# Kernel tuning notes

Hardware: AMD Instinct MI355X
Metric: run time of the kernel (lower is better)

The kernel has to match this reference:

```python
import jax, jax.numpy as jnp
import numpy as np
from jax import lax

B, R, C, K = 4, 512, 80, 100          # images, rois/img, fg classes, post_nms_top_k
NMS_TH, SCORE_TH = 0.3, 0.1
MEAN = jnp.zeros(4, jnp.float32)       # delta_mean
STD = jnp.ones(4, jnp.float32)         # delta_std
NEG = jnp.float32(-1e9)
DWH_CLIP = jnp.float32(4.135166556742356)  # log(1000/16), standard bbox_xform clip


def setup_inputs() -> dict:
    key = jax.random.key(0)
    k1, k2, k3, k4 = jax.random.split(key, 4)
    x1y1 = jax.random.uniform(k1, (B, R, 2), minval=0.0, maxval=800.0)
    wh = jax.random.uniform(k2, (B, R, 2), minval=16.0, maxval=220.0)
    batch_rois = jnp.concatenate([x1y1, jnp.minimum(x1y1 + wh, 1023.0)], axis=-1)
    bbox_score = jax.random.uniform(k3, (B * R, C + 1, 1, 1), dtype=jnp.float32)
    bbox_deltas = jax.random.normal(k4, (B * R, (C + 1) * 4, 1, 1), dtype=jnp.float32) * 0.2
    im_hw = jnp.full((B, 1, 1, 2), 1024, dtype=jnp.int32)
    return {"batch_rois": batch_rois, "bbox_score": bbox_score,
            "bbox_deltas": bbox_deltas, "im_hw": im_hw}


def _pairwise_iou(b):
    # b: [R, 4] (x1,y1,x2,y2) -> [R, R]
    area = (b[:, 2] - b[:, 0]) * (b[:, 3] - b[:, 1])
    lt = jnp.maximum(b[:, None, :2], b[None, :, :2])
    rb = jnp.minimum(b[:, None, 2:], b[None, :, 2:])
    wh = jnp.maximum(rb - lt, 0.0)
    inter = wh[..., 0] * wh[..., 1]
    return inter / (area[:, None] + area[None, :] - inter + 1e-9)


def _nms_one_class(boxes, scores):
    # boxes: [R,4], scores: [R] -> keep mask + score-sorted boxes/scores
    order = jnp.argsort(-scores)
    b = boxes[order]
    s = scores[order]
    iou = _pairwise_iou(b)  # [R, R]

    def body(sup, i):
        keep_i = jnp.logical_and(jnp.logical_not(sup[i]), s[i] > SCORE_TH)
        new = jnp.where(keep_i, jnp.logical_or(sup, iou[i] > NMS_TH), sup)
        new = new.at[i].set(sup[i])  # never self-suppress
        return new, keep_i

    _, keep = lax.scan(body, jnp.zeros(b.shape[0], bool), jnp.arange(b.shape[0]))
    return keep, b, s


def _decode(rois, deltas, hw):
    # rois: [R,4], deltas: [R,C,4], hw: [2] (h, w) -> decoded boxes [R,C,4]
    d = deltas * STD + MEAN
    w = rois[:, 2] - rois[:, 0]
    h = rois[:, 3] - rois[:, 1]
    cx = rois[:, 0] + 0.5 * w
    cy = rois[:, 1] + 0.5 * h
    dx, dy = d[..., 0], d[..., 1]
    dw = jnp.minimum(d[..., 2], DWH_CLIP)
    dh = jnp.minimum(d[..., 3], DWH_CLIP)
    pcx = dx * w[:, None] + cx[:, None]
    pcy = dy * h[:, None] + cy[:, None]
    pw = w[:, None] * jnp.exp(dw)
    ph = h[:, None] * jnp.exp(dh)
    x1 = jnp.clip(pcx - 0.5 * pw, 0.0, hw[1] - 1.0)
    y1 = jnp.clip(pcy - 0.5 * ph, 0.0, hw[0] - 1.0)
    x2 = jnp.clip(pcx + 0.5 * pw, 0.0, hw[1] - 1.0)
    y2 = jnp.clip(pcy + 0.5 * ph, 0.0, hw[0] - 1.0)
    return jnp.stack([x1, y1, x2, y2], axis=-1)


def reference(batch_rois, bbox_score, bbox_deltas, im_hw):
    scores = bbox_score.reshape(B, R, C + 1)[..., 1:]               # [B,R,C] (skip bg)
    deltas = bbox_deltas.reshape(B, R, C + 1, 4)[:, :, 1:, :]       # [B,R,C,4]
    hw = im_hw.reshape(B, 2).astype(jnp.float32)

    def per_image(rois, sc, dl, hw_i):
        boxes = _decode(rois, dl, hw_i)                              # [R,C,4]
        keep, bs, ss = jax.vmap(_nms_one_class)(
            jnp.swapaxes(boxes, 0, 1), sc.T)                         # [C,R]...
        cls = jnp.broadcast_to(jnp.arange(C, dtype=jnp.float32)[:, None], (C, R))
        flat_s = jnp.where(keep, ss, NEG).reshape(-1)                # [C*R]
        top_s, idx = lax.top_k(flat_s, K)
        tb = bs.reshape(-1, 4)[idx]
        tc = cls.reshape(-1)[idx]
        valid = top_s > NEG * 0.5
        row = jnp.concatenate([tb, top_s[:, None], tc[:, None]], axis=-1)  # [K,6]
        pad = jnp.concatenate([jnp.zeros((K, 5), jnp.float32),
                               -jnp.ones((K, 1), jnp.float32)], axis=-1)
        return jnp.where(valid[:, None], row, pad)

    return jax.vmap(per_image)(batch_rois, scores, deltas, hw)      # [B,K,6]
```

## Files before the change

kernel.cpp:

```cpp
#include <hip/hip_runtime.h>
#include <cstdint>

#define BB 4
#define RR 512
#define CC 80
#define KK 100
#define NMS_TH 0.3f
#define SCORE_TH 0.1f
#define DWH_CLIP 4.135166556742356f

typedef unsigned short u16;
typedef unsigned int u32;
typedef unsigned long long u64;

__device__ __forceinline__ u32 f32_sortable(float f) {
  u32 u = __float_as_uint(f);
  u32 mask = (u32)((int)u >> 31) | 0x80000000u;
  return u ^ mask;
}
__device__ __forceinline__ float sortable_to_f32(u32 s) {
  u32 u = (s & 0x80000000u) ? (s ^ 0x80000000u) : ~s;
  return __uint_as_float(u);
}

__global__ __launch_bounds__(512) void nms_fused(
    const float* __restrict__ rois,
    const float* __restrict__ scores,
    const float* __restrict__ deltas,
    const int*   __restrict__ im_hw,
    u64*   __restrict__ cand_key,
    float4* __restrict__ cand_box)
{
#pragma clang fp contract(off)
  const int bc = blockIdx.x;
  const int b = bc / CC, c = bc % CC;
  const int tid = threadIdx.x;
  const int lane = tid & 63, wv = tid >> 6;

  __shared__ u64    keyarr[RR];
  __shared__ float4 box_s[RR];
  __shared__ float  sco_s[RR];
  __shared__ u64    rmk_w[8 * 64];
  __shared__ u64    supacc_arr[8];
  __shared__ float4 kbox[KK];
  __shared__ float  ksc[KK];
  __shared__ float  karea[KK];
  __shared__ int    nkept_s;

  const float fh = (float)im_hw[b * 2 + 0] - 1.0f;
  const float fw = (float)im_hw[b * 2 + 1] - 1.0f;

  {
    const float sc = scores[(b * RR + tid) * (CC + 1) + (c + 1)];
    u64 v = ((u64)(~f32_sortable(sc)) << 32) | (u32)tid;
    const u32 t = (u32)tid;
    for (u32 kk = 2; kk <= RR; kk <<= 1) {
      for (u32 j = kk >> 1; j > 0; j >>= 1) {
        u64 p;
        if (j >= 64) {
          keyarr[t] = v;
          __syncthreads();
          p = keyarr[t ^ j];
          __syncthreads();
        } else {
          p = __shfl_xor(v, (int)j);
        }
        bool up = ((t & kk) == 0);
        bool lower = ((t & j) == 0);
        bool takemin = (up == lower);
        bool pless = (p < v);
        v = (takemin == pless) ? p : v;
      }
    }
    keyarr[t] = v;
  }
  __syncthreads();

  {
    const u64 kv = keyarr[tid];
    const int r = (int)(kv & 0xFFFFFFFFull);
    const float sc = sortable_to_f32(~(u32)(kv >> 32));
    const float4 roi = *(const float4*)&rois[(b * RR + r) * 4];
    const int base = (b * RR + r) * (CC + 1) + (c + 1);
    const float4 d = *(const float4*)&deltas[base * 4];

    float w  = roi.z - roi.x;
    float h  = roi.w - roi.y;
    float cx = roi.x + 0.5f * w;
    float cy = roi.y + 0.5f * h;
    float dw = fminf(d.z, DWH_CLIP);
    float dh = fminf(d.w, DWH_CLIP);
    float pcx = d.x * w + cx;
    float pcy = d.y * h + cy;
    float pw = w * expf(dw);
    float ph = h * expf(dh);
    float hx = 0.5f * pw, hy = 0.5f * ph;
    float x1 = fminf(fmaxf(pcx - hx, 0.0f), fw);
    float y1 = fminf(fmaxf(pcy - hy, 0.0f), fh);
    float x2 = fminf(fmaxf(pcx + hx, 0.0f), fw);
    float y2 = fminf(fmaxf(pcy + hy, 0.0f), fh);

    box_s[tid] = make_float4(x1, y1, x2, y2);
    sco_s[tid] = sc;
    if (tid == 0) nkept_s = 0;
  }
  __syncthreads();

  int nk = 0;
  for (int w = 0; w < 8 && nk < KK; ++w) {
    const float4 bxc = box_s[w * 64 + lane];
    const float ar = (bxc.z - bxc.x) * (bxc.w - bxc.y);
    const float areps = ar + 1e-9f;

    {
      u64 myrow = 0;
      #pragma unroll
      for (int jj = 0; jj < 8; ++jj) {
        const int j = wv * 8 + jj;
        const float4 cb = box_s[w * 64 + j];
        const float ca = (cb.z - cb.x) * (cb.w - cb.y);
        float iw = fminf(bxc.z, cb.z) - fmaxf(bxc.x, cb.x);
        float ih = fminf(bxc.w, cb.w) - fmaxf(bxc.y, cb.y);
        iw = fmaxf(iw, 0.0f);
        ih = fmaxf(ih, 0.0f);
        const float inter = iw * ih;
        const float S = ca + areps;
        bool yes = inter * 4.3333247f > S;
        const bool no = inter * 4.3333420f < S;
        if (__any(!(yes || no))) {
          const float denom = ((ca + ar) - inter) + 1e-9f;
          const bool pe = inter / denom > NMS_TH;
          yes = (yes || no) ? yes : pe;
        }
        myrow |= yes ? (1ull << j) : 0ull;
      }
      myrow &= ~((2ull << lane) - 1ull);
      rmk_w[wv * 64 + lane] = myrow;
    }

    {
      bool sup = false;
      for (int kx = wv; kx < nk; kx += 8) {
        const float4 kb = kbox[kx];
        const float ka = karea[kx];
        float iw = fminf(bxc.z, kb.z) - fmaxf(bxc.x, kb.x);
        float ih = fminf(bxc.w, kb.w) - fmaxf(bxc.y, kb.y);
        iw = fmaxf(iw, 0.0f);
        ih = fmaxf(ih, 0.0f);
        const float inter = iw * ih;
        const float S = ka + areps;
        bool yes = inter * 4.3333247f > S;
        const bool no = inter * 4.3333420f < S;
        if (__any(!(yes || no))) {
          const float denom = ((ka + ar) - inter) + 1e-9f;
          const bool pe = inter / denom > NMS_TH;
          yes = (yes || no) ? yes : pe;
        }
        sup = sup || yes;
      }
      const u64 bal = __ballot(sup);
      if (lane == 0) supacc_arr[wv] = bal;
    }
    __syncthreads();

    if (wv == 0) {
      u64 sup2 = supacc_arr[0];
      #pragma unroll
      for (int ww = 1; ww < 8; ++ww) sup2 |= supacc_arr[ww];
      u64 rm = rmk_w[lane];
      #pragma unroll
      for (int ww = 1; ww < 8; ++ww) rm |= rmk_w[ww * 64 + lane];
      const u32 rlo = (u32)rm, rhi = (u32)(rm >> 32);
      u64 todo = __ballot(sco_s[w * 64 + lane] > SCORE_TH) & ~sup2;
      int nkl = nk;
      while (todo) {
        const int i = __ffsll((long long)todo) - 1;
        if (lane == 0) {
          const float4 kb = box_s[w * 64 + i];
          kbox[nkl] = kb;
          ksc[nkl] = sco_s[w * 64 + i];
          karea[nkl] = (kb.z - kb.x) * (kb.w - kb.y);
        }
        ++nkl;
        if (nkl >= KK) break;
        const u32 rl = (u32)__builtin_amdgcn_readlane((int)rlo, i);
        const u32 rh = (u32)__builtin_amdgcn_readlane((int)rhi, i);
        todo &= ~((2ull << i) - 1ull);
        todo &= ~(((u64)rh << 32) | rl);
      }
      if (lane == 0) nkept_s = nkl;
    }
    __syncthreads();
    nk = nkept_s;
  }

  if (tid < KK) {
    const int kx = tid;
    u64 kv; float4 obx;
    if (kx < nk) {
      kv = ((u64)(~f32_sortable(ksc[kx])) << 32) | ((u64)(u32)c << 16) | (u32)kx;
      obx = kbox[kx];
    } else {
      kv = ((u64)(~f32_sortable(-1e9f)) << 32) | ((u64)(u32)c << 16) | (u32)kx;
      obx = make_float4(0.f, 0.f, 0.f, 0.f);
    }
    cand_key[bc * KK + kx] = kv;
    cand_box[bc * KK + kx] = obx;
  }
}

__device__ __forceinline__ void sort128(u64* smallkeys, int tid) {
  u64 v = (tid < 128) ? smallkeys[tid] : ~0ull;
  const u32 t = (u32)tid;
  for (u32 kk = 2; kk <= 128; kk <<= 1) {
    for (u32 j = kk >> 1; j > 0; j >>= 1) {
      if (j >= 64) {
        if (tid < 128) smallkeys[t] = v;
        __syncthreads();
        u64 p = (tid < 128) ? smallkeys[t ^ j] : ~0ull;
        __syncthreads();
        if (tid < 128) {
          bool up = ((t & kk) == 0);
          bool lower = ((t & j) == 0);
          bool takemin = (up == lower);
          bool pless = (p < v);
          v = (takemin == pless) ? p : v;
        }
      } else if (tid < 128) {
        u64 p = __shfl_xor(v, (int)j);
        bool up = ((t & kk) == 0);
        bool lower = ((t & j) == 0);
        bool takemin = (up == lower);
        bool pless = (p < v);
        v = (takemin == pless) ? p : v;
      }
    }
  }
  if (tid < 128) smallkeys[t] = v;
  __syncthreads();
}

__global__ __launch_bounds__(1024) void topk_select(
    const u64* __restrict__ cand_key,
    const float4* __restrict__ cand_box,
    float* __restrict__ out)
{
  const int b = blockIdx.x;
  const int tid = threadIdx.x;
  const int lane = tid & 63, wv = tid >> 6;
  const int N = CC * KK;
  const u64* __restrict__ keys_g = cand_key + (size_t)b * N;

  __shared__ u16 candA[CC * KK];
  __shared__ u16 candB[CC * KK];
  __shared__ u32 whist[16][256];
  __shared__ u32 bins[256];
  __shared__ u64 smallkeys[128];
  __shared__ int ncand_s, rank_s, q_s;
  __shared__ u32 cnt_s;

  if (tid == 0) { ncand_s = N; rank_s = KK - 1; }

  u16* cur = candA;
  u16* oth = candB;
  bool first = true;
  int d = 7;
  for (;;) {
    for (int t = tid; t < 16 * 256; t += 1024) ((u32*)whist)[t] = 0;
    __syncthreads();
    const int nc = first ? N : ncand_s;
    const int sh = d * 8;
    for (int t0 = 0; t0 < nc; t0 += 1024) {
      const int t = t0 + tid;
      if (t < nc) {
        const int idx = first ? t : (int)cur[t];
        u32 dig = (u32)((keys_g[idx] >> sh) & 0xFF);
        atomicAdd(&whist[wv][dig], 1u);
      }
    }
    __syncthreads();
    if (tid < 256) {
      u32 s = 0;
      #pragma unroll
      for (int w = 0; w < 16; ++w) s += whist[w][tid];
      bins[tid] = s;
    }
    __syncthreads();
    if (wv == 0) {
      u32 c0 = bins[lane * 4 + 0], c1 = bins[lane * 4 + 1];
      u32 c2 = bins[lane * 4 + 2], c3 = bins[lane * 4 + 3];
      u32 lsum = c0 + c1 + c2 + c3;
      u32 incl = lsum;
      #pragma unroll
      for (int off = 1; off < 64; off <<= 1) {
        u32 v = __shfl_up(incl, off);
        if (lane >= off) incl += v;
      }
      u32 excl = incl - lsum;
      int rk = rank_s;
      u32 s0 = excl, s1 = excl + c0, s2 = s1 + c1, s3 = s2 + c2;
      int q = -1; u32 nr = 0;
      if (rk >= (int)s0 && rk < (int)(s0 + c0)) { q = lane * 4 + 0; nr = rk - s0; }
      else if (rk >= (int)s1 && rk < (int)(s1 + c1)) { q = lane * 4 + 1; nr = rk - s1; }
      else if (rk >= (int)s2 && rk < (int)(s2 + c2)) { q = lane * 4 + 2; nr = rk - s2; }
      else if (rk >= (int)s3 && rk < (int)(s3 + c3)) { q = lane * 4 + 3; nr = rk - s3; }
      if (q >= 0) { q_s = q; rank_s = (int)nr; }
    }
    if (tid == 0) cnt_s = 0;
    __syncthreads();
    const int q = q_s;
    for (int t0 = 0; t0 < nc; t0 += 1024) {
      const int t = t0 + tid;
      int idx = 0; bool m = false;
      if (t < nc) {
        idx = first ? t : (int)cur[t];
        m = ((int)((keys_g[idx] >> sh) & 0xFF) == q);
      }
      u64 bal = __ballot(m);
      u32 base = 0;
      if (lane == 0 && bal) base = atomicAdd(&cnt_s, (u32)__popcll(bal));
      base = __shfl(base, 0);
      if (m) oth[base + (u32)__popcll(bal & ((1ull << lane) - 1ull))] = (u16)idx;
    }
    __syncthreads();
    if (tid == 0) ncand_s = (int)cnt_s;
    { u16* tmp = cur; cur = oth; oth = tmp; }
    first = false;
    __syncthreads();
    if (ncand_s <= 128 || d == 0) break;
    --d;
  }

  u64 T;
  const int nc2 = ncand_s;
  if (nc2 == 1) {
    T = keys_g[cur[0]];
  } else {
    if (tid < 128) smallkeys[tid] = (tid < nc2) ? keys_g[cur[tid]] : ~0ull;
    __syncthreads();
    sort128(smallkeys, tid);
    T = smallkeys[rank_s];
    __syncthreads();
  }

  if (tid == 0) cnt_s = 0;
  if (tid < 128) smallkeys[tid] = ~0ull;
  __syncthreads();
  for (int t0 = 0; t0 < N; t0 += 1024) {
    const int t = t0 + tid;
    u64 k = 0; bool m = false;
    if (t < N) { k = keys_g[t]; m = (k <= T); }
    u64 bal = __ballot(m);
    u32 base = 0;
    if (lane == 0 && bal) base = atomicAdd(&cnt_s, (u32)__popcll(bal));
    base = __shfl(base, 0);
    if (m) {
      u32 p = base + (u32)__popcll(bal & ((1ull << lane) - 1ull));
      if (p < 128) smallkeys[p] = k;
    }
  }
  __syncthreads();

  sort128(smallkeys, tid);

  if (tid < KK) {
    const u64 kv = smallkeys[tid];
    const float s = sortable_to_f32(~(u32)(kv >> 32));
    float x1 = 0.f, y1 = 0.f, x2 = 0.f, y2 = 0.f, so = 0.f, cf = -1.0f;
    if (s > -5.0e8f) {
      int c = (int)((kv >> 16) & 0xFFFFull);
      int k = (int)(kv & 0xFFFFull);
      float4 bx = cand_box[((size_t)b * CC + c) * KK + k];
      x1 = bx.x; y1 = bx.y; x2 = bx.z; y2 = bx.w;
      so = s; cf = (float)c;
    }
    float* o = out + ((size_t)b * KK + tid) * 6;
    o[0] = x1; o[1] = y1; o[2] = x2; o[3] = y2; o[4] = so; o[5] = cf;
  }
}

extern "C" void kernel_launch(void* const* d_in, const int* in_sizes, int n_in,
                              void* d_out, int out_size, void* d_ws, size_t ws_size,
                              hipStream_t stream) {
  (void)in_sizes; (void)n_in; (void)out_size; (void)ws_size;
  const float* rois   = (const float*)d_in[0];
  const float* scores = (const float*)d_in[1];
  const float* deltas = (const float*)d_in[2];
  const int*   im_hw  = (const int*)d_in[3];

  char* ws = (char*)d_ws;
  u64*    cand_key = (u64*)ws;
  float4* cand_box = (float4*)(ws + 256000);

  nms_fused<<<BB * CC, 512, 0, stream>>>(rois, scores, deltas, im_hw,
                                         cand_key, cand_box);
  topk_select<<<BB, 1024, 0, stream>>>(cand_key, cand_box, (float*)d_out);
}
```

Baseline: 64.06 us.

## Replace radix-select top-k with a single-wave 80-way sorted-list merge

The second kernel previously ran a multi-pass radix select with histograms, compaction and two bitonic sorts over 8000 candidate keys per image. It now relies on each class's candidates already being in score order and runs a single 64-lane wave that merges the 80 sorted lists. Each step takes a wave-wide shuffle minimum and advances the winning list head, using a small per-lane register prefetch. The NMS kernel's bitonic sort also gets a double-buffered shared array, which removes one barrier per cross-wave stage. The trade-off is 100 serial merge steps with dependent global loads on a single wave per image.

```diff
diff --git a/kernel.cpp b/kernel.cpp
--- a/kernel.cpp
+++ b/kernel.cpp
@@ -37,7 +37,7 @@
   const int tid = threadIdx.x;
   const int lane = tid & 63, wv = tid >> 6;
 
-  __shared__ u64    keyarr[RR];
+  __shared__ u64    keyarr[2 * RR];
   __shared__ float4 box_s[RR];
   __shared__ float  sco_s[RR];
   __shared__ u64    rmk_w[8 * 64];
@@ -54,14 +54,16 @@
     const float sc = scores[(b * RR + tid) * (CC + 1) + (c + 1)];
     u64 v = ((u64)(~f32_sortable(sc)) << 32) | (u32)tid;
     const u32 t = (u32)tid;
+    u32 pp = 0;
     for (u32 kk = 2; kk <= RR; kk <<= 1) {
       for (u32 j = kk >> 1; j > 0; j >>= 1) {
         u64 p;
         if (j >= 64) {
-          keyarr[t] = v;
+          u64* buf = keyarr + (pp & 1) * RR;
+          buf[t] = v;
           __syncthreads();
-          p = keyarr[t ^ j];
-          __syncthreads();
+          p = buf[t ^ j];
+          ++pp;
         } else {
           p = __shfl_xor(v, (int)j);
         }
@@ -209,172 +211,58 @@
   }
 }
 
-__device__ __forceinline__ void sort128(u64* smallkeys, int tid) {
-  u64 v = (tid < 128) ? smallkeys[tid] : ~0ull;
-  const u32 t = (u32)tid;
-  for (u32 kk = 2; kk <= 128; kk <<= 1) {
-    for (u32 j = kk >> 1; j > 0; j >>= 1) {
-      if (j >= 64) {
-        if (tid < 128) smallkeys[t] = v;
-        __syncthreads();
-        u64 p = (tid < 128) ? smallkeys[t ^ j] : ~0ull;
-        __syncthreads();
-        if (tid < 128) {
-          bool up = ((t & kk) == 0);
-          bool lower = ((t & j) == 0);
-          bool takemin = (up == lower);
-          bool pless = (p < v);
-          v = (takemin == pless) ? p : v;
-        }
-      } else if (tid < 128) {
-        u64 p = __shfl_xor(v, (int)j);
-        bool up = ((t & kk) == 0);
-        bool lower = ((t & j) == 0);
-        bool takemin = (up == lower);
-        bool pless = (p < v);
-        v = (takemin == pless) ? p : v;
-      }
-    }
-  }
-  if (tid < 128) smallkeys[t] = v;
-  __syncthreads();
-}
-
-__global__ __launch_bounds__(1024) void topk_select(
+__global__ __launch_bounds__(64) void topk_merge(
     const u64* __restrict__ cand_key,
     const float4* __restrict__ cand_box,
     float* __restrict__ out)
 {
   const int b = blockIdx.x;
-  const int tid = threadIdx.x;
-  const int lane = tid & 63, wv = tid >> 6;
-  const int N = CC * KK;
-  const u64* __restrict__ keys_g = cand_key + (size_t)b * N;
-
-  __shared__ u16 candA[CC * KK];
-  __shared__ u16 candB[CC * KK];
-  __shared__ u32 whist[16][256];
-  __shared__ u32 bins[256];
-  __shared__ u64 smallkeys[128];
-  __shared__ int ncand_s, rank_s, q_s;
-  __shared__ u32 cnt_s;
-
-  if (tid == 0) { ncand_s = N; rank_s = KK - 1; }
-
-  u16* cur = candA;
-  u16* oth = candB;
-  bool first = true;
-  int d = 7;
-  for (;;) {
-    for (int t = tid; t < 16 * 256; t += 1024) ((u32*)whist)[t] = 0;
-    __syncthreads();
-    const int nc = first ? N : ncand_s;
-    const int sh = d * 8;
-    for (int t0 = 0; t0 < nc; t0 += 1024) {
-      const int t = t0 + tid;
-      if (t < nc) {
-        const int idx = first ? t : (int)cur[t];
-        u32 dig = (u32)((keys_g[idx] >> sh) & 0xFF);
-        atomicAdd(&whist[wv][dig], 1u);
-      }
-    }
-    __syncthreads();
-    if (tid < 256) {
-      u32 s = 0;
-      #pragma unroll
-      for (int w = 0; w < 16; ++w) s += whist[w][tid];
-      bins[tid] = s;
-    }
-    __syncthreads();
-    if (wv == 0) {
-      u32 c0 = bins[lane * 4 + 0], c1 = bins[lane * 4 + 1];
-      u32 c2 = bins[lane * 4 + 2], c3 = bins[lane * 4 + 3];
-      u32 lsum = c0 + c1 + c2 + c3;
-      u32 incl = lsum;
-      #pragma unroll
-      for (int off = 1; off < 64; off <<= 1) {
-        u32 v = __shfl_up(incl, off);
-        if (lane >= off) incl += v;
-      }
-      u32 excl = incl - lsum;
-      int rk = rank_s;
-      u32 s0 = excl, s1 = excl + c0, s2 = s1 + c1, s3 = s2 + c2;
-      int q = -1; u32 nr = 0;
-      if (rk >= (int)s0 && rk < (int)(s0 + c0)) { q = lane * 4 + 0; nr = rk - s0; }
-      else if (rk >= (int)s1 && rk < (int)(s1 + c1)) { q = lane * 4 + 1; nr = rk - s1; }
-      else if (rk >= (int)s2 && rk < (int)(s2 + c2)) { q = lane * 4 + 2; nr = rk - s2; }
-      else if (rk >= (int)s3 && rk < (int)(s3 + c3)) { q = lane * 4 + 3; nr = rk - s3; }
-      if (q >= 0) { q_s = q; rank_s = (int)nr; }
-    }
-    if (tid == 0) cnt_s = 0;
-    __syncthreads();
-    const int q = q_s;
-    for (int t0 = 0; t0 < nc; t0 += 1024) {
-      const int t = t0 + tid;
-      int idx = 0; bool m = false;
-      if (t < nc) {
-        idx = first ? t : (int)cur[t];
-        m = ((int)((keys_g[idx] >> sh) & 0xFF) == q);
-      }
-      u64 bal = __ballot(m);
-      u32 base = 0;
-      if (lane == 0 && bal) base = atomicAdd(&cnt_s, (u32)__popcll(bal));
-      base = __shfl(base, 0);
-      if (m) oth[base + (u32)__popcll(bal & ((1ull << lane) - 1ull))] = (u16)idx;
-    }
-    __syncthreads();
-    if (tid == 0) ncand_s = (int)cnt_s;
-    { u16* tmp = cur; cur = oth; oth = tmp; }
-    first = false;
-    __syncthreads();
-    if (ncand_s <= 128 || d == 0) break;
-    --d;
-  }
-
-  u64 T;
-  const int nc2 = ncand_s;
-  if (nc2 == 1) {
-    T = keys_g[cur[0]];
-  } else {
-    if (tid < 128) smallkeys[tid] = (tid < nc2) ? keys_g[cur[tid]] : ~0ull;
-    __syncthreads();
-    sort128(smallkeys, tid);
-    T = smallkeys[rank_s];
-    __syncthreads();
-  }
-
-  if (tid == 0) cnt_s = 0;
-  if (tid < 128) smallkeys[tid] = ~0ull;
+  const int lane = threadIdx.x;
+
+  __shared__ u64 pop_s[KK];
+
+  const u64* __restrict__ baseA = cand_key + ((size_t)b * CC + lane) * KK;
+  const bool hasB = lane < (CC - 64);
+  const u64* __restrict__ baseB = cand_key + ((size_t)b * CC + 64 + lane) * KK;
+
+  int posA = 0, posB = 0;
+  u64 a0 = baseA[0], a1 = baseA[1], a2 = baseA[2];
+  u64 b0 = hasB ? baseB[0] : ~0ull;
+  u64 b1 = hasB ? baseB[1] : ~0ull;
+  u64 b2 = hasB ? baseB[2] : ~0ull;
+
+  for (int t = 0; t < KK; ++t) {
+    u64 m = (a0 < b0) ? a0 : b0;
+    #pragma unroll
+    for (int off = 32; off >= 1; off >>= 1) {
+      const u64 p = __shfl_xor(m, off);
+      m = (p < m) ? p : m;
+    }
+    if (lane == 0) pop_s[t] = m;
+    if (a0 == m) {
+      a0 = a1; a1 = a2;
+      a2 = (posA + 3 < KK) ? baseA[posA + 3] : ~0ull;
+      ++posA;
+    } else if (b0 == m) {
+      b0 = b1; b1 = b2;
+      b2 = (posB + 3 < KK) ? baseB[posB + 3] : ~0ull;
+      ++posB;
+    }
+  }
   __syncthreads();
-  for (int t0 = 0; t0 < N; t0 += 1024) {
-    const int t = t0 + tid;
-    u64 k = 0; bool m = false;
-    if (t < N) { k = keys_g[t]; m = (k <= T); }
-    u64 bal = __ballot(m);
-    u32 base = 0;
-    if (lane == 0 && bal) base = atomicAdd(&cnt_s, (u32)__popcll(bal));
-    base = __shfl(base, 0);
-    if (m) {
-      u32 p = base + (u32)__popcll(bal & ((1ull << lane) - 1ull));
-      if (p < 128) smallkeys[p] = k;
-    }
-  }
-  __syncthreads();
-
-  sort128(smallkeys, tid);
-
-  if (tid < KK) {
-    const u64 kv = smallkeys[tid];
+
+  for (int t = lane; t < KK; t += 64) {
+    const u64 kv = pop_s[t];
     const float s = sortable_to_f32(~(u32)(kv >> 32));
     float x1 = 0.f, y1 = 0.f, x2 = 0.f, y2 = 0.f, so = 0.f, cf = -1.0f;
     if (s > -5.0e8f) {
-      int c = (int)((kv >> 16) & 0xFFFFull);
-      int k = (int)(kv & 0xFFFFull);
-      float4 bx = cand_box[((size_t)b * CC + c) * KK + k];
+      const int c = (int)((kv >> 16) & 0xFFFFull);
+      const int k = (int)(kv & 0xFFFFull);
+      const float4 bx = cand_box[((size_t)b * CC + c) * KK + k];
       x1 = bx.x; y1 = bx.y; x2 = bx.z; y2 = bx.w;
       so = s; cf = (float)c;
     }
-    float* o = out + ((size_t)b * KK + tid) * 6;
+    float* o = out + ((size_t)b * KK + t) * 6;
     o[0] = x1; o[1] = y1; o[2] = x2; o[3] = y2; o[4] = so; o[5] = cf;
   }
 }
@@ -394,5 +282,5 @@
 
   nms_fused<<<BB * CC, 512, 0, stream>>>(rois, scores, deltas, im_hw,
                                          cand_key, cand_box);
-  topk_select<<<BB, 1024, 0, stream>>>(cand_key, cand_box, (float*)d_out);
-}
+  topk_merge<<<BB, 64, 0, stream>>>(cand_key, cand_box, (float*)d_out);
+}
```

Measured after the change: 81.92 us. +27.9%, slower.

## Overlap next-chunk IoU mask with serial NMS scan and double-buffer bitonic sort

Applied to the files above, without the earlier changes.

Restructures the per-class NMS loop so wave 0 runs the serial greedy scan for chunk w while waves 1-7 compute the intra-chunk IoU mask and suppression by previously kept boxes for chunk w+1. A small follow-up pass then checks chunk w+1 against only the boxes kept during chunk w. The bitonic sort also ping-pongs between two shared buffers, which removes one barrier per cross-wave step. This adds an extra barrier per chunk and more shared memory, and shifts mask work from 8 waves to 7.

```diff
diff --git a/kernel.cpp b/kernel.cpp
--- a/kernel.cpp
+++ b/kernel.cpp
@@ -22,6 +22,23 @@
   u32 u = (s & 0x80000000u) ? (s ^ 0x80000000u) : ~s;
   return __uint_as_float(u);
 }
+
+#define IOU_YES(bxc, ar, areps, cb, ca, yes)                                  \
+  {                                                                           \
+    float iw = fminf((bxc).z, (cb).z) - fmaxf((bxc).x, (cb).x);               \
+    float ih = fminf((bxc).w, (cb).w) - fmaxf((bxc).y, (cb).y);               \
+    iw = fmaxf(iw, 0.0f);                                                     \
+    ih = fmaxf(ih, 0.0f);                                                     \
+    const float inter = iw * ih;                                              \
+    const float S = (ca) + (areps);                                           \
+    yes = inter * 4.3333247f > S;                                             \
+    const bool no_ = inter * 4.3333420f < S;                                  \
+    if (__any(!(yes || no_))) {                                               \
+      const float denom = (((ca) + (ar)) - inter) + 1e-9f;                    \
+      const bool pe_ = inter / denom > NMS_TH;                                \
+      yes = (yes || no_) ? yes : pe_;                                         \
+    }                                                                         \
+  }
 
 __global__ __launch_bounds__(512) void nms_fused(
     const float* __restrict__ rois,
@@ -37,11 +54,12 @@
   const int tid = threadIdx.x;
   const int lane = tid & 63, wv = tid >> 6;
 
-  __shared__ u64    keyarr[RR];
+  __shared__ u64    keyarr[2 * RR];
   __shared__ float4 box_s[RR];
   __shared__ float  sco_s[RR];
-  __shared__ u64    rmk_w[8 * 64];
-  __shared__ u64    supacc_arr[8];
+  __shared__ u64    rmk2[2][7 * 64];
+  __shared__ u64    supPre[2][8];
+  __shared__ u64    deltaS[2][8];
   __shared__ float4 kbox[KK];
   __shared__ float  ksc[KK];
   __shared__ float  karea[KK];
@@ -54,14 +72,16 @@
     const float sc = scores[(b * RR + tid) * (CC + 1) + (c + 1)];
     u64 v = ((u64)(~f32_sortable(sc)) << 32) | (u32)tid;
     const u32 t = (u32)tid;
+    u32 pp = 0;
     for (u32 kk = 2; kk <= RR; kk <<= 1) {
       for (u32 j = kk >> 1; j > 0; j >>= 1) {
         u64 p;
         if (j >= 64) {
-          keyarr[t] = v;
+          u64* buf = keyarr + (pp & 1) * RR;
+          buf[t] = v;
           __syncthreads();
-          p = keyarr[t ^ j];
-          __syncthreads();
+          p = buf[t ^ j];
+          ++pp;
         } else {
           p = __shfl_xor(v, (int)j);
         }
@@ -106,73 +126,42 @@
   }
   __syncthreads();
 
+  if (wv >= 1) {
+    const float4 bxr = box_s[lane];
+    const float ar = (bxr.z - bxr.x) * (bxr.w - bxr.y);
+    const float areps = ar + 1e-9f;
+    u64 myrow = 0;
+    for (int j = wv - 1; j < 64; j += 7) {
+      const float4 cb = box_s[j];
+      const float ca = (cb.z - cb.x) * (cb.w - cb.y);
+      bool yes;
+      IOU_YES(bxr, ar, areps, cb, ca, yes);
+      myrow |= yes ? (1ull << j) : 0ull;
+    }
+    myrow &= ~((2ull << lane) - 1ull);
+    rmk2[0][(wv - 1) * 64 + lane] = myrow;
+  }
+  if (tid < 8)  supPre[0][tid] = 0ull;
+  if (tid >= 8 && tid < 16) deltaS[0][tid - 8] = 0ull;
+  __syncthreads();
+
   int nk = 0;
-  for (int w = 0; w < 8 && nk < KK; ++w) {
-    const float4 bxc = box_s[w * 64 + lane];
-    const float ar = (bxc.z - bxc.x) * (bxc.w - bxc.y);
-    const float areps = ar + 1e-9f;
-
-    {
-      u64 myrow = 0;
+  for (int w = 0; w < 8; ++w) {
+    const int p = w & 1, pn = p ^ 1;
+    const int nk_base = nk;
+
+    if (wv == 0) {
+      u64 sup2 = deltaS[p][0];
       #pragma unroll
-      for (int jj = 0; jj < 8; ++jj) {
-        const int j = wv * 8 + jj;
-        const float4 cb = box_s[w * 64 + j];
-        const float ca = (cb.z - cb.x) * (cb.w - cb.y);
-        float iw = fminf(bxc.z, cb.z) - fmaxf(bxc.x, cb.x);
-        float ih = fminf(bxc.w, cb.w) - fmaxf(bxc.y, cb.y);
-        iw = fmaxf(iw, 0.0f);
-        ih = fmaxf(ih, 0.0f);
-        const float inter = iw * ih;
-        const float S = ca + areps;
-        bool yes = inter * 4.3333247f > S;
-        const bool no = inter * 4.3333420f < S;
-        if (__any(!(yes || no))) {
-          const float denom = ((ca + ar) - inter) + 1e-9f;
-          const bool pe = inter / denom > NMS_TH;
-          yes = (yes || no) ? yes : pe;
-        }
-        myrow |= yes ? (1ull << j) : 0ull;
-      }
-      myrow &= ~((2ull << lane) - 1ull);
-      rmk_w[wv * 64 + lane] = myrow;
-    }
-
-    {
-      bool sup = false;
-      for (int kx = wv; kx < nk; kx += 8) {
-        const float4 kb = kbox[kx];
-        const float ka = karea[kx];
-        float iw = fminf(bxc.z, kb.z) - fmaxf(bxc.x, kb.x);
-        float ih = fminf(bxc.w, kb.w) - fmaxf(bxc.y, kb.y);
-        iw = fmaxf(iw, 0.0f);
-        ih = fmaxf(ih, 0.0f);
-        const float inter = iw * ih;
-        const float S = ka + areps;
-        bool yes = inter * 4.3333247f > S;
-        const bool no = inter * 4.3333420f < S;
-        if (__any(!(yes || no))) {
-          const float denom = ((ka + ar) - inter) + 1e-9f;
-          const bool pe = inter / denom > NMS_TH;
-          yes = (yes || no) ? yes : pe;
-        }
-        sup = sup || yes;
-      }
-      const u64 bal = __ballot(sup);
-      if (lane == 0) supacc_arr[wv] = bal;
-    }
-    __syncthreads();
-
-    if (wv == 0) {
-      u64 sup2 = supacc_arr[0];
+      for (int s = 1; s < 8; ++s) sup2 |= deltaS[p][s];
       #pragma unroll
-      for (int ww = 1; ww < 8; ++ww) sup2 |= supacc_arr[ww];
-      u64 rm = rmk_w[lane];
+      for (int s = 0; s < 7; ++s) sup2 |= supPre[p][s];
+      u64 rm = rmk2[p][lane];
       #pragma unroll
-      for (int ww = 1; ww < 8; ++ww) rm |= rmk_w[ww * 64 + lane];
+      for (int s = 1; s < 7; ++s) rm |= rmk2[p][s * 64 + lane];
       const u32 rlo = (u32)rm, rhi = (u32)(rm >> 32);
       u64 todo = __ballot(sco_s[w * 64 + lane] > SCORE_TH) & ~sup2;
-      int nkl = nk;
+      int nkl = nk_base;
       while (todo) {
         const int i = __ffsll((long long)todo) - 1;
         if (lane == 0) {
@@ -189,15 +178,59 @@
         todo &= ~(((u64)rh << 32) | rl);
       }
       if (lane == 0) nkept_s = nkl;
+    } else if (w < 7) {
+      const float4 bxr = box_s[(w + 1) * 64 + lane];
+      const float ar = (bxr.z - bxr.x) * (bxr.w - bxr.y);
+      const float areps = ar + 1e-9f;
+      u64 myrow = 0;
+      for (int j = wv - 1; j < 64; j += 7) {
+        const float4 cb = box_s[(w + 1) * 64 + j];
+        const float ca = (cb.z - cb.x) * (cb.w - cb.y);
+        bool yes;
+        IOU_YES(bxr, ar, areps, cb, ca, yes);
+        myrow |= yes ? (1ull << j) : 0ull;
+      }
+      myrow &= ~((2ull << lane) - 1ull);
+      rmk2[pn][(wv - 1) * 64 + lane] = myrow;
+
+      bool sup = false;
+      for (int kx = wv - 1; kx < nk_base; kx += 7) {
+        const float4 kb = kbox[kx];
+        const float ka = karea[kx];
+        bool yes;
+        IOU_YES(bxr, ar, areps, kb, ka, yes);
+        sup = sup || yes;
+      }
+      const u64 bal = __ballot(sup);
+      if (lane == 0) supPre[pn][wv - 1] = bal;
     }
     __syncthreads();
     nk = nkept_s;
-  }
-
+    if (nk >= KK || w == 7) break;
+
+    {
+      const float4 bxc = box_s[(w + 1) * 64 + lane];
+      const float ar = (bxc.z - bxc.x) * (bxc.w - bxc.y);
+      const float areps = ar + 1e-9f;
+      bool sup = false;
+      for (int kx = nk_base + wv; kx < nk; kx += 8) {
+        const float4 kb = kbox[kx];
+        const float ka = karea[kx];
+        bool yes;
+        IOU_YES(bxc, ar, areps, kb, ka, yes);
+        sup = sup || yes;
+      }
+      const u64 bal = __ballot(sup);
+      if (lane == 0) deltaS[pn][wv] = bal;
+    }
+    __syncthreads();
+  }
+
+  const int nko = min(nk, KK);
   if (tid < KK) {
     const int kx = tid;
     u64 kv; float4 obx;
-    if (kx < nk) {
+    if (kx < nko) {
       kv = ((u64)(~f32_sortable(ksc[kx])) << 32) | ((u64)(u32)c << 16) | (u32)kx;
       obx = kbox[kx];
     } else {
```

Measured after the change: 65.87 us. 2.8% more time.
